# Optimization experiments

Hardware: AMD Instinct MI355X
Metric: run time of the kernel (lower is better)

## Reference

```python
import jax, jax.numpy as jnp
import numpy as np


def setup_inputs() -> dict:
    key = jax.random.key(0)
    k1, k2 = jax.random.split(key)
    B, D, H, W = 4, 32, 32, 16
    logits = jax.random.normal(k1, (B, D, H, W), dtype=jnp.float32)
    # binary segmentation targets (0/1), cast to float as in the torch module
    targets = jax.random.randint(k2, (B, D, H, W), 0, 2).astype(jnp.float32)
    return {"logits": logits, "targets": targets}


def reference(logits, targets):
    B = logits.shape[0]
    spatial = logits.shape[1:]
    V = int(np.prod(spatial))
    # Voxel coordinates of the full grid (row-major, same order as torch.nonzero).
    grids = jnp.meshgrid(*[jnp.arange(s) for s in spatial], indexing="ij")
    coords = jnp.stack(grids, axis=-1).reshape(V, len(spatial)).astype(jnp.float32)  # [V, ndim]
    # Shared squared pairwise distance matrix between all grid voxels: [V, V].
    # ||p - t||^2 = ||p||^2 + ||t||^2 - 2 p.t ; max over masked pairs then sqrt
    # equals max of cdist over masked pairs (sqrt is monotone).
    sq = jnp.sum(coords * coords, axis=1)  # [V]
    d2 = sq[:, None] + sq[None, :] - 2.0 * (coords @ coords.T)  # [V, V]

    probs = jax.nn.sigmoid(logits).reshape(B, V)
    pmask = probs > 0.5                     # pred foreground voxels  [B, V]
    tmask = targets.reshape(B, V) > 0.5     # target foreground voxels [B, V]
    neg_inf = jnp.float32(-jnp.inf)

    def per_sample(masks):
        pm, tm = masks
        # max over target voxels for each pred voxel, then max over pred voxels.
        # Note: torch code takes max over the FULL cdist matrix in both
        # directions; both equal the max pairwise distance, so one pass suffices.
        row = jnp.max(jnp.where(tm[None, :], d2, neg_inf), axis=1)  # [V]
        m = jnp.max(jnp.where(pm, row, neg_inf))
        valid = jnp.any(pm) & jnp.any(tm)
        return jnp.where(valid, jnp.sqrt(jnp.maximum(m, 0.0)), jnp.inf)

    # sequential over batch to avoid materializing [B, V, V]
    hd = jax.lax.map(per_sample, (pmask, tmask))  # [B]
    return jnp.mean(hd)
```

## Files before the change

kernel.cpp:

```cpp
#include <hip/hip_runtime.h>
#include <math.h>

#define NB 4
#define ND 32
#define NH 32
#define NW 16
#define COLS_PER_SAMPLE (ND * NH)
#define VPS (COLS_PER_SAMPLE * NW)
#define NBLK 1024

__global__ __launch_bounds__(256) void hd_fused(
    const float* __restrict__ logits, const float* __restrict__ targets,
    int* __restrict__ bmax) {
    __shared__ int2 s_pe[64];
    __shared__ int2 s_te[64];
    __shared__ int s_red[4];

    int bid = blockIdx.x;
    int s = bid >> 8;
    int pchunk = (bid >> 4) & 15;
    int tchunk = bid & 15;
    int tid = threadIdx.x;

    const float4* pl = (const float4*)(logits  + s * VPS + pchunk * 1024);
    const float4* tl = (const float4*)(targets + s * VPS + tchunk * 1024);
    float4 pv = pl[tid];
    float4 tv = tl[tid];
    int q = (tid & 3) * 4;

    int pmn = 1000, pmx = -1;
    if (pv.x > 0.0f) { pmn = q;              pmx = q;     }
    if (pv.y > 0.0f) { pmn = min(pmn, q + 1); pmx = q + 1; }
    if (pv.z > 0.0f) { pmn = min(pmn, q + 2); pmx = q + 2; }
    if (pv.w > 0.0f) { pmn = min(pmn, q + 3); pmx = q + 3; }
    int tmn = 1000, tmx = -1;
    if (tv.x > 0.5f) { tmn = q;              tmx = q;     }
    if (tv.y > 0.5f) { tmn = min(tmn, q + 1); tmx = q + 1; }
    if (tv.z > 0.5f) { tmn = min(tmn, q + 2); tmx = q + 2; }
    if (tv.w > 0.5f) { tmn = min(tmn, q + 3); tmx = q + 3; }

#pragma unroll
    for (int m = 1; m <= 2; m <<= 1) {
        pmn = min(pmn, __shfl_xor(pmn, m, 64));
        pmx = max(pmx, __shfl_xor(pmx, m, 64));
        tmn = min(tmn, __shfl_xor(tmn, m, 64));
        tmx = max(tmx, __shfl_xor(tmx, m, 64));
    }
    if ((tid & 3) == 0) {
        s_pe[tid >> 2] = make_int2(pmn, pmx);
        s_te[tid >> 2] = make_int2(tmn, tmx);
    }
    __syncthreads();

    int pl_idx = tid >> 2;
    int2 pe = s_pe[pl_idx];
    int best = -1;
    if (pe.y >= 0) {
        int pcol = pchunk * 64 + pl_idx;
        int pd = pcol >> 5, ph = pcol & 31;
        int tb0 = (tid & 3) * 16;
#pragma unroll
        for (int i = 0; i < 16; ++i) {
            int tl_idx = tb0 + i;
            int2 te = s_te[tl_idx];
            if (te.y < 0) continue;
            int tcol = tchunk * 64 + tl_idx;
            int td = tcol >> 5, th = tcol & 31;
            int dd = pd - td, dh = ph - th;
            int basew = dd * dd + dh * dh;
            int a = pe.x - te.x, c = pe.x - te.y;
            int d = pe.y - te.x, e = pe.y - te.y;
            int m = max(max(a * a, c * c), max(d * d, e * e));
            best = max(best, basew + m);
        }
    }

#pragma unroll
    for (int m = 32; m >= 1; m >>= 1) best = max(best, __shfl_xor(best, m, 64));
    if ((tid & 63) == 0) s_red[tid >> 6] = best;
    __syncthreads();
    if (tid == 0)
        bmax[bid] = max(max(s_red[0], s_red[1]), max(s_red[2], s_red[3]));
}

__global__ __launch_bounds__(256) void hd_final(const int* __restrict__ bmax,
                                                float* __restrict__ out) {
    __shared__ float s_val[4];
    int tid = threadIdx.x;
    int w = tid >> 6;
    int lane = tid & 63;
    const int* p = bmax + w * 256;
    int m = max(max(p[lane], p[lane + 64]), max(p[lane + 128], p[lane + 192]));
#pragma unroll
    for (int k = 32; k >= 1; k >>= 1) m = max(m, __shfl_xor(m, k, 64));
    if (lane == 0) s_val[w] = (m < 0) ? INFINITY : sqrtf((float)m);
    __syncthreads();
    if (tid == 0) {
        float ssum = s_val[0] + s_val[1] + s_val[2] + s_val[3];
        out[0] = ssum * (1.0f / NB);
    }
}

extern "C" void kernel_launch(void* const* d_in, const int* in_sizes, int n_in,
                              void* d_out, int out_size, void* d_ws, size_t ws_size,
                              hipStream_t stream) {
    const float* logits  = (const float*)d_in[0];
    const float* targets = (const float*)d_in[1];
    float* out = (float*)d_out;
    int* bmax = (int*)d_ws;

    hd_fused<<<NBLK, 256, 0, stream>>>(logits, targets, bmax);
    hd_final<<<1, 256, 0, stream>>>(bmax, out);
}
```

Baseline: 11.52 us.

## Fuse final reduction via last-block atomic counter and retile to 128 blocks

Merges the two kernels into one: each block writes its partial max, bumps a global atomic counter, and the last block to finish does the final per-sample max, sqrt and mean. The grid shrinks from 1024 to 128 blocks, each covering 256 pred columns by 128 target columns, and each thread builds a 16-bit column mask with ffs/clz instead of the shuffle-based min/max. This removes a second kernel launch and the redundant loads across many tiny blocks, at the cost of longer per-thread loops and fewer blocks to spread across the GPU. The counter uses modulo arithmetic so it does not need to be reset between calls, which assumes the workspace starts at zero.

```diff
diff --git a/kernel.cpp b/kernel.cpp
--- a/kernel.cpp
+++ b/kernel.cpp
@@ -5,99 +5,102 @@
 #define ND 32
 #define NH 32
 #define NW 16
-#define COLS_PER_SAMPLE (ND * NH)
-#define VPS (COLS_PER_SAMPLE * NW)
-#define NBLK 1024
+#define CPS (ND * NH)
+#define VPS (CPS * NW)
+#define NBLK 128
+#define PCOLS 256
+#define TCOLS 128
 
-__global__ __launch_bounds__(256) void hd_fused(
+__global__ __launch_bounds__(256) void hd_one(
     const float* __restrict__ logits, const float* __restrict__ targets,
-    int* __restrict__ bmax) {
-    __shared__ int2 s_pe[64];
-    __shared__ int2 s_te[64];
+    int* bmax, unsigned* cnt, float* __restrict__ out) {
+    __shared__ int2 s_te[TCOLS];
     __shared__ int s_red[4];
+    __shared__ int s_win;
 
     int bid = blockIdx.x;
-    int s = bid >> 8;
-    int pchunk = (bid >> 4) & 15;
-    int tchunk = bid & 15;
+    int s = bid >> 5;
+    int pchunk = (bid >> 3) & 3;
+    int tchunk = bid & 7;
     int tid = threadIdx.x;
 
-    const float4* pl = (const float4*)(logits  + s * VPS + pchunk * 1024);
-    const float4* tl = (const float4*)(targets + s * VPS + tchunk * 1024);
-    float4 pv = pl[tid];
-    float4 tv = tl[tid];
-    int q = (tid & 3) * 4;
+    int pcol = pchunk * PCOLS + tid;
+    const float4* pp = (const float4*)(logits + s * VPS + pcol * NW);
+    unsigned pmsk = 0;
+#pragma unroll
+    for (int j = 0; j < 4; ++j) {
+        float4 v = pp[j];
+        pmsk |= (v.x > 0.0f ? 1u : 0u) << (4 * j);
+        pmsk |= (v.y > 0.0f ? 1u : 0u) << (4 * j + 1);
+        pmsk |= (v.z > 0.0f ? 1u : 0u) << (4 * j + 2);
+        pmsk |= (v.w > 0.0f ? 1u : 0u) << (4 * j + 3);
+    }
+    int pe_min = pmsk ? (__ffs(pmsk) - 1) : 1000;
+    int pe_max = pmsk ? (31 - __clz(pmsk)) : -1;
 
-    int pmn = 1000, pmx = -1;
-    if (pv.x > 0.0f) { pmn = q;              pmx = q;     }
-    if (pv.y > 0.0f) { pmn = min(pmn, q + 1); pmx = q + 1; }
-    if (pv.z > 0.0f) { pmn = min(pmn, q + 2); pmx = q + 2; }
-    if (pv.w > 0.0f) { pmn = min(pmn, q + 3); pmx = q + 3; }
-    int tmn = 1000, tmx = -1;
-    if (tv.x > 0.5f) { tmn = q;              tmx = q;     }
-    if (tv.y > 0.5f) { tmn = min(tmn, q + 1); tmx = q + 1; }
-    if (tv.z > 0.5f) { tmn = min(tmn, q + 2); tmx = q + 2; }
-    if (tv.w > 0.5f) { tmn = min(tmn, q + 3); tmx = q + 3; }
-
+    if (tid < TCOLS) {
+        int tcol = tchunk * TCOLS + tid;
+        const float4* tp = (const float4*)(targets + s * VPS + tcol * NW);
+        unsigned tmsk = 0;
 #pragma unroll
-    for (int m = 1; m <= 2; m <<= 1) {
-        pmn = min(pmn, __shfl_xor(pmn, m, 64));
-        pmx = max(pmx, __shfl_xor(pmx, m, 64));
-        tmn = min(tmn, __shfl_xor(tmn, m, 64));
-        tmx = max(tmx, __shfl_xor(tmx, m, 64));
-    }
-    if ((tid & 3) == 0) {
-        s_pe[tid >> 2] = make_int2(pmn, pmx);
-        s_te[tid >> 2] = make_int2(tmn, tmx);
+        for (int j = 0; j < 4; ++j) {
+            float4 v = tp[j];
+            tmsk |= (v.x > 0.5f ? 1u : 0u) << (4 * j);
+            tmsk |= (v.y > 0.5f ? 1u : 0u) << (4 * j + 1);
+            tmsk |= (v.z > 0.5f ? 1u : 0u) << (4 * j + 2);
+            tmsk |= (v.w > 0.5f ? 1u : 0u) << (4 * j + 3);
+        }
+        s_te[tid] = make_int2(tmsk ? (__ffs(tmsk) - 1) : 1000,
+                              tmsk ? (31 - __clz(tmsk)) : -1);
     }
     __syncthreads();
 
-    int pl_idx = tid >> 2;
-    int2 pe = s_pe[pl_idx];
+    int pd = pcol >> 5, ph = pcol & 31;
+    int td0 = (tchunk * TCOLS) >> 5;
     int best = -1;
-    if (pe.y >= 0) {
-        int pcol = pchunk * 64 + pl_idx;
-        int pd = pcol >> 5, ph = pcol & 31;
-        int tb0 = (tid & 3) * 16;
-#pragma unroll
-        for (int i = 0; i < 16; ++i) {
-            int tl_idx = tb0 + i;
-            int2 te = s_te[tl_idx];
-            if (te.y < 0) continue;
-            int tcol = tchunk * 64 + tl_idx;
-            int td = tcol >> 5, th = tcol & 31;
-            int dd = pd - td, dh = ph - th;
-            int basew = dd * dd + dh * dh;
-            int a = pe.x - te.x, c = pe.x - te.y;
-            int d = pe.y - te.x, e = pe.y - te.y;
-            int m = max(max(a * a, c * c), max(d * d, e * e));
-            best = max(best, basew + m);
-        }
+#pragma unroll 8
+    for (int i = 0; i < TCOLS; ++i) {
+        int2 te = s_te[i];
+        int dd = pd - (td0 + (i >> 5));
+        int dh = ph - (i & 31);
+        int b2 = __mul24(dd, dd) + __mul24(dh, dh);
+        int a = pe_min - te.x, c = pe_min - te.y;
+        int d = pe_max - te.x, e = pe_max - te.y;
+        int q = max(max(__mul24(a, a), __mul24(c, c)),
+                    max(__mul24(d, d), __mul24(e, e)));
+        int cand = b2 + q;
+        best = (te.y >= 0) ? max(best, cand) : best;
     }
+    if (pe_max < 0) best = -1;
 
 #pragma unroll
     for (int m = 32; m >= 1; m >>= 1) best = max(best, __shfl_xor(best, m, 64));
     if ((tid & 63) == 0) s_red[tid >> 6] = best;
     __syncthreads();
-    if (tid == 0)
-        bmax[bid] = max(max(s_red[0], s_red[1]), max(s_red[2], s_red[3]));
-}
 
-__global__ __launch_bounds__(256) void hd_final(const int* __restrict__ bmax,
-                                                float* __restrict__ out) {
-    __shared__ float s_val[4];
-    int tid = threadIdx.x;
-    int w = tid >> 6;
-    int lane = tid & 63;
-    const int* p = bmax + w * 256;
-    int m = max(max(p[lane], p[lane + 64]), max(p[lane + 128], p[lane + 192]));
+    if (tid == 0) {
+        int mx = max(max(s_red[0], s_red[1]), max(s_red[2], s_red[3]));
+        __hip_atomic_store(&bmax[bid], mx, __ATOMIC_RELAXED,
+                           __HIP_MEMORY_SCOPE_AGENT);
+        asm volatile("s_waitcnt vmcnt(0)" ::: "memory");
+        unsigned old = atomicAdd(cnt, 1u);
+        s_win = (((old + 1u) & (NBLK - 1u)) == 0u);
+    }
+    __syncthreads();
+
+    if (s_win && tid < 64) {
+        int g = tid >> 4, j = tid & 15;
+        int m1 = __hip_atomic_load(&bmax[g * 32 + j], __ATOMIC_RELAXED,
+                                   __HIP_MEMORY_SCOPE_AGENT);
+        int m2 = __hip_atomic_load(&bmax[g * 32 + 16 + j], __ATOMIC_RELAXED,
+                                   __HIP_MEMORY_SCOPE_AGENT);
+        int m = max(m1, m2);
 #pragma unroll
-    for (int k = 32; k >= 1; k >>= 1) m = max(m, __shfl_xor(m, k, 64));
-    if (lane == 0) s_val[w] = (m < 0) ? INFINITY : sqrtf((float)m);
-    __syncthreads();
-    if (tid == 0) {
-        float ssum = s_val[0] + s_val[1] + s_val[2] + s_val[3];
-        out[0] = ssum * (1.0f / NB);
+        for (int k = 8; k >= 1; k >>= 1) m = max(m, __shfl_xor(m, k, 64));
+        float hd = (m < 0) ? INFINITY : sqrtf((float)m);
+        float ssum = hd + __shfl_xor(hd, 16, 64);
+        ssum += __shfl_xor(ssum, 32, 64);
+        if (tid == 0) out[0] = ssum * (1.0f / NB);
     }
 }
 
@@ -107,8 +110,9 @@
     const float* logits  = (const float*)d_in[0];
     const float* targets = (const float*)d_in[1];
     float* out = (float*)d_out;
+
     int* bmax = (int*)d_ws;
+    unsigned* cnt = (unsigned*)((char*)d_ws + NBLK * sizeof(int));
 
-    hd_fused<<<NBLK, 256, 0, stream>>>(logits, targets, bmax);
-    hd_final<<<1, 256, 0, stream>>>(bmax, out);
+    hd_one<<<NBLK, 256, 0, stream>>>(logits, targets, bmax, cnt, out);
 }
```

Result: slower. 14.37 us (+24.8%).
